# Kernel tuning notes

Measured on AMD Instinct MI355X. Metric: run time of the kernel, lower is better.

Reference implementation:

```python
import jax, jax.numpy as jnp
import numpy as np

D_MODEL = 1024
N_HEADS = 16
D_HEAD = D_MODEL // N_HEADS
D_FF = 4096
EPS = 1e-5


def layernorm(x, gamma, beta):
    mu = jnp.mean(x, axis=-1, keepdims=True)
    var = jnp.var(x, axis=-1, keepdims=True)
    return (x - mu) * jax.lax.rsqrt(var + EPS) * gamma + beta


def setup_inputs() -> dict:
    key = jax.random.key(0)
    ks = jax.random.split(key, 16)
    B, T = 4, 2048
    s = 1.0 / np.sqrt(D_MODEL)
    sf = 1.0 / np.sqrt(D_FF)
    return {
        "x": jax.random.normal(ks[0], (B, T, D_MODEL), jnp.float32),
        "gate_score": jax.random.uniform(ks[1], (B,), jnp.float32),
        "Wq": jax.random.normal(ks[2], (D_MODEL, D_MODEL), jnp.float32) * s,
        "bq": jnp.zeros((D_MODEL,), jnp.float32),
        "Wk": jax.random.normal(ks[3], (D_MODEL, D_MODEL), jnp.float32) * s,
        "bk": jnp.zeros((D_MODEL,), jnp.float32),
        "Wv": jax.random.normal(ks[4], (D_MODEL, D_MODEL), jnp.float32) * s,
        "bv": jnp.zeros((D_MODEL,), jnp.float32),
        "Wo": jax.random.normal(ks[5], (D_MODEL, D_MODEL), jnp.float32) * s,
        "bo": jnp.zeros((D_MODEL,), jnp.float32),
        "W1": jax.random.normal(ks[6], (D_MODEL, D_FF), jnp.float32) * s,
        "b1": jnp.zeros((D_FF,), jnp.float32),
        "W2": jax.random.normal(ks[7], (D_FF, D_MODEL), jnp.float32) * sf,
        "b2": jnp.zeros((D_MODEL,), jnp.float32),
        "gamma1": jnp.ones((D_MODEL,), jnp.float32),
        "beta1": jnp.zeros((D_MODEL,), jnp.float32),
        "gamma2": jnp.ones((D_MODEL,), jnp.float32),
        "beta2": jnp.zeros((D_MODEL,), jnp.float32),
    }


def reference(x, gate_score, Wq, bq, Wk, bk, Wv, bv, Wo, bo,
              W1, b1, W2, b2, gamma1, beta1, gamma2, beta2):
    B, T, C = x.shape
    # --- attention sub-block (pre-norm) ---
    h = layernorm(x, gamma1, beta1)
    Q = (h @ Wq + bq).reshape(B, T, N_HEADS, D_HEAD).transpose(0, 2, 1, 3)
    K = (h @ Wk + bk).reshape(B, T, N_HEADS, D_HEAD).transpose(0, 2, 1, 3)
    V = (h @ Wv + bv).reshape(B, T, N_HEADS, D_HEAD).transpose(0, 2, 1, 3)
    scores = jnp.einsum("bhqd,bhkd->bhqk", Q, K) / np.sqrt(D_HEAD)
    causal = jnp.tril(jnp.ones((T, T), dtype=bool))  # True = keep
    scores = jnp.where(causal, scores, -jnp.inf)
    attn = jax.nn.softmax(scores, axis=-1)
    ctx = jnp.einsum("bhqk,bhkd->bhqd", attn, V)
    ctx = ctx.transpose(0, 2, 1, 3).reshape(B, T, C)
    attn_out = ctx @ Wo + bo
    x1 = x + attn_out
    # --- FFN sub-block (pre-norm) ---
    h2 = layernorm(x1, gamma2, beta2)
    ff = jax.nn.gelu(h2 @ W1 + b1, approximate=False) @ W2 + b2
    x2 = x1 + ff
    # --- gated residual ---
    g = gate_score[:, None, None]
    return x + g * (x2 - x)
```

## Files before the change

### kernel.cpp

```cpp
#include <hip/hip_runtime.h>
#include <hip/hip_bf16.h>
#include <cmath>

typedef unsigned short u16;
typedef __attribute__((ext_vector_type(8))) short short8;
typedef __attribute__((ext_vector_type(4))) float f32x4;

#define DM 1024
#define NH 16
#define DH 64
#define DFF 4096
#define BB 4
#define TT 2048
#define MROWS (BB*TT)

__device__ __forceinline__ float bu2f(u16 u) {
    union { float f; unsigned v; } c; c.v = ((unsigned)u) << 16; return c.f;
}
__device__ __forceinline__ u16 f2bu(float f) {
    __hip_bfloat16 h = __float2bfloat16(f);
    union { __hip_bfloat16 h; u16 u; } c; c.h = h; return c.u;
}
__device__ __forceinline__ void async_copy16(const u16* g, u16* l) {
    __builtin_amdgcn_global_load_lds((const __attribute__((address_space(1))) void*)g,
                                     (__attribute__((address_space(3))) void*)l, 16, 0, 0);
}

__global__ void ln_kernel(const float* __restrict__ x, const float* __restrict__ gamma,
                          const float* __restrict__ beta, u16* __restrict__ out)
{
    int row = blockIdx.x;
    int tid = threadIdx.x;
    float4 v4 = ((const float4*)(x + (size_t)row * DM))[tid];
    float v[4] = { v4.x, v4.y, v4.z, v4.w };
    float s = v[0] + v[1] + v[2] + v[3];
    float ss = v[0]*v[0] + v[1]*v[1] + v[2]*v[2] + v[3]*v[3];
    #pragma unroll
    for (int o = 32; o > 0; o >>= 1) { s += __shfl_down(s, o); ss += __shfl_down(ss, o); }
    __shared__ float red[8];
    int w = tid >> 6;
    if ((tid & 63) == 0) { red[w] = s; red[4 + w] = ss; }
    __syncthreads();
    s  = red[0] + red[1] + red[2] + red[3];
    ss = red[4] + red[5] + red[6] + red[7];
    float mu  = s * (1.0f / DM);
    float var = ss * (1.0f / DM) - mu * mu;
    float rstd = rsqrtf(var + 1e-5f);
    float4 g4 = ((const float4*)gamma)[tid];
    float4 b4 = ((const float4*)beta)[tid];
    float g[4] = { g4.x, g4.y, g4.z, g4.w };
    float b[4] = { b4.x, b4.y, b4.z, b4.w };
    ushort4 o4;
    u16* op = (u16*)&o4;
    #pragma unroll
    for (int i = 0; i < 4; i++) op[i] = f2bu((v[i] - mu) * rstd * g[i] + b[i]);
    ((ushort4*)(out + (size_t)row * DM))[tid] = o4;
}

__global__ void transpose4_f2b(const float* __restrict__ w0, const float* __restrict__ w1,
                               const float* __restrict__ w2, const float* __restrict__ w3,
                               u16* __restrict__ outQKV, u16* __restrict__ outO)
{
    __shared__ u16 tile[32][33];
    const float* in = (blockIdx.z == 0) ? w0 : (blockIdx.z == 1) ? w1
                     : (blockIdx.z == 2) ? w2 : w3;
    u16* out = (blockIdx.z < 3) ? (outQKV + (size_t)blockIdx.z * DM * DM) : outO;
    int bx = blockIdx.x * 32;
    int by = blockIdx.y * 32;
    int tx = threadIdx.x, ty = threadIdx.y;
    #pragma unroll
    for (int i = 0; i < 32; i += 8)
        tile[ty + i][tx] = f2bu(in[(size_t)(by + ty + i) * DM + bx + tx]);
    __syncthreads();
    #pragma unroll
    for (int i = 0; i < 32; i += 8)
        out[(size_t)(bx + ty + i) * DM + by + tx] = tile[tx][ty + i];
}

__global__ void transpose_f2b(const float* __restrict__ in, u16* __restrict__ out,
                              int R, int C)
{
    __shared__ u16 tile[32][33];
    int bx = blockIdx.x * 32;
    int by = blockIdx.y * 32;
    int tx = threadIdx.x, ty = threadIdx.y;
    #pragma unroll
    for (int i = 0; i < 32; i += 8)
        tile[ty + i][tx] = f2bu(in[(size_t)(by + ty + i) * C + bx + tx]);
    __syncthreads();
    #pragma unroll
    for (int i = 0; i < 32; i += 8)
        out[(size_t)(bx + ty + i) * R + by + tx] = tile[tx][ty + i];
}

#define BM 128
#define BN 128
#define BK 64

template<int EPI>
__global__ void gemm_bt(
    const u16* __restrict__ A, const u16* __restrict__ Bt,
    const float* __restrict__ bias, const float* __restrict__ bias2,
    const float* __restrict__ bias3, void* __restrict__ Cv,
    const float* __restrict__ res, const float* __restrict__ x0,
    const float* __restrict__ gate, int M, int N, int K)
{
    __shared__ __align__(16) u16 As[BM * BK];
    __shared__ __align__(16) u16 Bs[BN * BK];
    int tid = threadIdx.x;
    int lane = tid & 63, wave = tid >> 6;
    int wm = (wave & 1) * 64, wn = (wave >> 1) * 64;
    int lm = lane & 15, quad = lane >> 4;
    size_t row0 = (size_t)blockIdx.x * BM;
    size_t col0 = (size_t)blockIdx.y * BN;

    int sr = tid >> 3;
    int scol = (((tid & 7) ^ (sr & 7)) * 8);
    const u16* Ag = A  + (row0 + sr) * (size_t)K + scol;
    const u16* Bg = Bt + (col0 + sr) * (size_t)K + scol;
    u16* Asl = As + tid * 8;
    u16* Bsl = Bs + tid * 8;

    int fc0 = ((0 * 4 + quad) ^ (lm & 7)) * 8;
    int fc1 = ((1 * 4 + quad) ^ (lm & 7)) * 8;

    f32x4 acc[4][4];
    #pragma unroll
    for (int i = 0; i < 4; i++)
        #pragma unroll
        for (int j = 0; j < 4; j++)
            acc[i][j] = (f32x4){0.f, 0.f, 0.f, 0.f};

    for (int k0 = 0; k0 < K; k0 += BK) {
        __syncthreads();
        async_copy16(Ag + k0,                  Asl);
        async_copy16(Ag + (size_t)32 * K + k0, Asl + 32 * BK);
        async_copy16(Ag + (size_t)64 * K + k0, Asl + 64 * BK);
        async_copy16(Ag + (size_t)96 * K + k0, Asl + 96 * BK);
        async_copy16(Bg + k0,                  Bsl);
        async_copy16(Bg + (size_t)32 * K + k0, Bsl + 32 * BK);
        async_copy16(Bg + (size_t)64 * K + k0, Bsl + 64 * BK);
        async_copy16(Bg + (size_t)96 * K + k0, Bsl + 96 * BK);
        __syncthreads();
        #pragma unroll
        for (int ks = 0; ks < 2; ks++) {
            int fc = ks ? fc1 : fc0;
            short8 af[4], bfr[4];
            #pragma unroll
            for (int t = 0; t < 4; t++) {
                af[t]  = *(const short8*)&As[(wm + t * 16 + lm) * BK + fc];
                bfr[t] = *(const short8*)&Bs[(wn + t * 16 + lm) * BK + fc];
            }
            #pragma unroll
            for (int mt = 0; mt < 4; mt++)
                #pragma unroll
                for (int nt = 0; nt < 4; nt++)
                    acc[mt][nt] = __builtin_amdgcn_mfma_f32_16x16x32_bf16(
                        af[mt], bfr[nt], acc[mt][nt], 0, 0, 0);
        }
    }

    u16*   C16 = (u16*)Cv;
    float* Cf  = (float*)Cv;

    const float* bb = bias;
    size_t csub = 0;
    if (EPI == 0 && bias2 != nullptr) {
        size_t cbase = col0 + wn;
        if (cbase >= 2048)      { bb = bias3; csub = 2048; }
        else if (cbase >= 1024) { bb = bias2; csub = 1024; }
    }

    #pragma unroll
    for (int mt = 0; mt < 4; mt++) {
        #pragma unroll
        for (int nt = 0; nt < 4; nt++) {
            #pragma unroll
            for (int r = 0; r < 4; r++) {
                size_t row = row0 + wm + mt * 16 + quad * 4 + r;
                size_t col = col0 + wn + nt * 16 + lm;
                size_t idx = row * (size_t)N + col;
                float v = acc[mt][nt][r] + bb[col - csub];
                if (EPI == 0) {
                    C16[idx] = f2bu(v);
                } else if (EPI == 1) {
                    Cf[idx] = v + res[idx];
                } else if (EPI == 2) {
                    v = 0.5f * v * (1.0f + erff(v * 0.70710678118f));
                    C16[idx] = f2bu(v);
                } else {
                    float xv  = x0[idx];
                    float x1v = res[idx];
                    float g   = gate[row >> 11];
                    Cf[idx] = xv + g * (x1v + v - xv);
                }
            }
        }
    }
}

#define AVS 72

__global__ __launch_bounds__(256, 4) void attn_mfma(
    const u16* __restrict__ QKV, u16* __restrict__ ctx)
{
    __shared__ __align__(16) u16 Kl[64][AVS];
    __shared__ __align__(16) u16 Vt[64][AVS];
    __shared__ __align__(16) u16 Pl[4][16][AVS];

    const int LD = 3 * DM;
    int tid = threadIdx.x, lane = tid & 63, w = tid >> 6;
    int lm = lane & 15, quad = lane >> 4;

    int bi = blockIdx.x;
    int pair = bi & 15, h = (bi >> 4) & 15, b = bi >> 8;
    int t1 = 31 - pair, t2 = pair;

    const size_t hoff = (size_t)h * DH;
    const u16* Qp = QKV + (size_t)b * TT * LD + hoff;
    const u16* Kp = Qp + DM;
    const u16* Vp = Qp + 2 * DM;

    short8 aqA[2], aqB[2];
    #pragma unroll
    for (int dc = 0; dc < 2; dc++) {
        aqA[dc] = *(const short8*)(Qp + (size_t)(t1 * 64 + w * 16 + lm) * LD + dc * 32 + quad * 8);
        aqB[dc] = *(const short8*)(Qp + (size_t)(t2 * 64 + w * 16 + lm) * LD + dc * 32 + quad * 8);
    }

    int kkey = tid & 63, kdim = (tid >> 6) * 16;
    int vkey = (tid & 31) * 2, vdim = (tid >> 5) * 8;

    const u16* kb0 = Kp + (size_t)kkey * LD + kdim;
    const u16* vb0 = Vp + (size_t)vkey * LD + vdim;
    const u16* vb1 = Vp + (size_t)(vkey + 1) * LD + vdim;

    const float sc = 0.18033688011f;
    const float FM = 24.0f;
    const short s1 = (short)0x3F80;
    const short8 ones = (short8){s1, s1, s1, s1, s1, s1, s1, s1};

    uint4 kr0 = *(const uint4*)(kb0);
    uint4 kr1 = *(const uint4*)(kb0 + 8);
    uint4 vr0 = *(const uint4*)(vb0);
    uint4 vr1 = *(const uint4*)(vb1);

    #pragma unroll
    for (int ti = 0; ti < 2; ti++) {
        int tcur = (ti == 0) ? t1 : t2;
        int nch = tcur + 1;
        int q0 = tcur * 64;
        int qw = q0 + w * 16;
        short8 a0 = (ti == 0) ? aqA[0] : aqB[0];
        short8 a1 = (ti == 0) ? aqA[1] : aqB[1];
        int qv = qw + lm;

        f32x4 o[4], o5;
        #pragma unroll
        for (int ds = 0; ds < 4; ds++) o[ds] = (f32x4){0.f, 0.f, 0.f, 0.f};
        o5 = (f32x4){0.f, 0.f, 0.f, 0.f};

        for (int c = 0; c < nch; c++) {
            int kb = c * 64;
            __syncthreads();
            *(uint4*)&Kl[kkey][kdim]     = kr0;
            *(uint4*)&Kl[kkey][kdim + 8] = kr1;
            {
                const u16* p0 = (const u16*)&vr0;
                const u16* p1 = (const u16*)&vr1;
                #pragma unroll
                for (int j = 0; j < 8; j++) {
                    ushort2 pk = { p0[j], p1[j] };
                    *(ushort2*)&Vt[vdim + j][vkey] = pk;
                }
            }
            __syncthreads();

            {
                size_t offn = (c + 1 < nch) ? (size_t)(c + 1) * 64 * LD : 0;
                kr0 = *(const uint4*)(kb0 + offn);
                kr1 = *(const uint4*)(kb0 + offn + 8);
                vr0 = *(const uint4*)(vb0 + offn);
                vr1 = *(const uint4*)(vb1 + offn);
            }

            f32x4 s[4];
            #pragma unroll
            for (int ks = 0; ks < 4; ks++) s[ks] = (f32x4){0.f, 0.f, 0.f, 0.f};
            #pragma unroll
            for (int ks = 0; ks < 4; ks++) {
                short8 k0 = *(const short8*)&Kl[ks * 16 + lm][quad * 8];
                short8 k1 = *(const short8*)&Kl[ks * 16 + lm][32 + quad * 8];
                s[ks] = __builtin_amdgcn_mfma_f32_16x16x32_bf16(k0, a0, s[ks], 0, 0, 0);
                s[ks] = __builtin_amdgcn_mfma_f32_16x16x32_bf16(k1, a1, s[ks], 0, 0, 0);
            }

            bool mz = (kb + 63 > qw);
            #pragma unroll
            for (int ks = 0; ks < 4; ks++) {
                int kbase = kb + ks * 16 + quad * 4;
                ushort4 pk;
                u16* pp = (u16*)&pk;
                #pragma unroll
                for (int r = 0; r < 4; r++) {
                    float v = s[ks][r] * sc - FM;
                    if (mz && (kbase + r > qv)) v = -INFINITY;
                    pp[r] = f2bu(exp2f(v));
                }
                *(ushort4*)&Pl[w][lm][ks * 16 + quad * 4] = pk;
            }

            #pragma unroll
            for (int kc = 0; kc < 2; kc++) {
                short8 ap = *(const short8*)&Pl[w][lm][kc * 32 + quad * 8];
                #pragma unroll
                for (int ds = 0; ds < 4; ds++) {
                    short8 bv = *(const short8*)&Vt[ds * 16 + lm][kc * 32 + quad * 8];
                    o[ds] = __builtin_amdgcn_mfma_f32_16x16x32_bf16(ap, bv, o[ds], 0, 0, 0);
                }
                o5 = __builtin_amdgcn_mfma_f32_16x16x32_bf16(ap, ones, o5, 0, 0, 0);
            }
        }

        float inv[4];
        #pragma unroll
        for (int r = 0; r < 4; r++) inv[r] = 1.0f / o5[r];
        #pragma unroll
        for (int ds = 0; ds < 4; ds++)
            #pragma unroll
            for (int r = 0; r < 4; r++) {
                size_t row = (size_t)(b * TT + qw + quad * 4 + r);
                ctx[row * DM + hoff + ds * 16 + lm] = f2bu(o[ds][r] * inv[r]);
            }
    }
}

extern "C" void kernel_launch(void* const* d_in, const int* in_sizes, int n_in,
                              void* d_out, int out_size, void* d_ws, size_t ws_size,
                              hipStream_t stream)
{
    const float* x    = (const float*)d_in[0];
    const float* gate = (const float*)d_in[1];
    const float* Wq   = (const float*)d_in[2];
    const float* bq   = (const float*)d_in[3];
    const float* Wk   = (const float*)d_in[4];
    const float* bk   = (const float*)d_in[5];
    const float* Wv   = (const float*)d_in[6];
    const float* bv   = (const float*)d_in[7];
    const float* Wo   = (const float*)d_in[8];
    const float* bo   = (const float*)d_in[9];
    const float* W1   = (const float*)d_in[10];
    const float* b1   = (const float*)d_in[11];
    const float* W2   = (const float*)d_in[12];
    const float* b2   = (const float*)d_in[13];
    const float* gamma1 = (const float*)d_in[14];
    const float* beta1  = (const float*)d_in[15];
    const float* gamma2 = (const float*)d_in[16];
    const float* beta2  = (const float*)d_in[17];
    float* out = (float*)d_out;

    char* ws = (char*)d_ws;
    const size_t MB = 1024 * 1024;
    u16* WtQKV = (u16*)(ws + 0 * MB);
    u16* WtO   = (u16*)(ws + 6 * MB);
    u16* Wt1   = (u16*)(ws + 8 * MB);
    u16* Wt2   = (u16*)(ws + 16 * MB);
    u16* h     = (u16*)(ws + 24 * MB);
    u16* ctx   = (u16*)(ws + 24 * MB);
    u16* QKVb  = (u16*)(ws + 40 * MB);
    float* x1  = (float*)(ws + 40 * MB);
    u16* h2    = (u16*)(ws + 72 * MB);
    u16* ff    = (u16*)(ws + 88 * MB);

    dim3 tb(32, 8);
    transpose4_f2b<<<dim3(32, 32, 4), tb, 0, stream>>>(Wq, Wk, Wv, Wo, WtQKV, WtO);
    transpose_f2b<<<dim3(DFF / 32, DM / 32), tb, 0, stream>>>(W1, Wt1, DM, DFF);
    transpose_f2b<<<dim3(DM / 32, DFF / 32), tb, 0, stream>>>(W2, Wt2, DFF, DM);

    ln_kernel<<<MROWS, 256, 0, stream>>>(x, gamma1, beta1, h);

    gemm_bt<0><<<dim3(MROWS / BM, 3 * DM / BN), 256, 0, stream>>>(
        h, WtQKV, bq, bk, bv, QKVb, nullptr, nullptr, nullptr, MROWS, 3 * DM, DM);

    attn_mfma<<<BB * NH * 16, 256, 0, stream>>>(QKVb, ctx);

    gemm_bt<1><<<dim3(MROWS / BM, DM / BN), 256, 0, stream>>>(
        ctx, WtO, bo, nullptr, nullptr, x1, x, nullptr, nullptr, MROWS, DM, DM);

    ln_kernel<<<MROWS, 256, 0, stream>>>(x1, gamma2, beta2, h2);

    gemm_bt<2><<<dim3(MROWS / BM, DFF / BN), 256, 0, stream>>>(
        h2, Wt1, b1, nullptr, nullptr, ff, nullptr, nullptr, nullptr, MROWS, DFF, DM);

    gemm_bt<3><<<dim3(MROWS / BM, DM / BN), 256, 0, stream>>>(
        ff, Wt2, b2, nullptr, nullptr, out, x1, x, gate, MROWS, DM, DFF);
}
```

Measured before the change: 537.4 us.

## Share K/V tile loads between both query tiles in causal attention

Each attention block handles a pair of query tiles (t1 = 31-pair and t2 = pair). It now walks the key chunks once for the longer tile and runs the shorter tile's compute on the same staged K/V tiles while c <= t2, instead of looping over K/V twice. This removes the redundant global loads, LDS staging and barriers for the shorter tile. The cost is two sets of output accumulators held live, which raises register pressure and may lower occupancy.

Result: slower. 794.9 us (+47.9%).

```diff
diff --git a/kernel.cpp b/kernel.cpp
--- a/kernel.cpp
+++ b/kernel.cpp
@@ -221,11 +221,14 @@
     const u16* Kp = Qp + DM;
     const u16* Vp = Qp + 2 * DM;
 
-    short8 aqA[2], aqB[2];
+    int qw1 = t1 * 64 + w * 16, qv1 = qw1 + lm;
+    int qw2 = t2 * 64 + w * 16, qv2 = qw2 + lm;
+
+    short8 aq1[2], aq2[2];
     #pragma unroll
     for (int dc = 0; dc < 2; dc++) {
-        aqA[dc] = *(const short8*)(Qp + (size_t)(t1 * 64 + w * 16 + lm) * LD + dc * 32 + quad * 8);
-        aqB[dc] = *(const short8*)(Qp + (size_t)(t2 * 64 + w * 16 + lm) * LD + dc * 32 + quad * 8);
+        aq1[dc] = *(const short8*)(Qp + (size_t)(qw1 + lm) * LD + dc * 32 + quad * 8);
+        aq2[dc] = *(const short8*)(Qp + (size_t)(qw2 + lm) * LD + dc * 32 + quad * 8);
     }
 
     int kkey = tid & 63, kdim = (tid >> 6) * 16;
@@ -240,97 +243,109 @@
     const short s1 = (short)0x3F80;
     const short8 ones = (short8){s1, s1, s1, s1, s1, s1, s1, s1};
 
+    f32x4 o1[4], o2[4], l1, l2;
+    #pragma unroll
+    for (int ds = 0; ds < 4; ds++) {
+        o1[ds] = (f32x4){0.f, 0.f, 0.f, 0.f};
+        o2[ds] = (f32x4){0.f, 0.f, 0.f, 0.f};
+    }
+    l1 = (f32x4){0.f, 0.f, 0.f, 0.f};
+    l2 = (f32x4){0.f, 0.f, 0.f, 0.f};
+
     uint4 kr0 = *(const uint4*)(kb0);
     uint4 kr1 = *(const uint4*)(kb0 + 8);
     uint4 vr0 = *(const uint4*)(vb0);
     uint4 vr1 = *(const uint4*)(vb1);
 
-    #pragma unroll
-    for (int ti = 0; ti < 2; ti++) {
-        int tcur = (ti == 0) ? t1 : t2;
-        int nch = tcur + 1;
-        int q0 = tcur * 64;
-        int qw = q0 + w * 16;
-        short8 a0 = (ti == 0) ? aqA[0] : aqB[0];
-        short8 a1 = (ti == 0) ? aqA[1] : aqB[1];
-        int qv = qw + lm;
-
-        f32x4 o[4], o5;
-        #pragma unroll
-        for (int ds = 0; ds < 4; ds++) o[ds] = (f32x4){0.f, 0.f, 0.f, 0.f};
-        o5 = (f32x4){0.f, 0.f, 0.f, 0.f};
-
-        for (int c = 0; c < nch; c++) {
-            int kb = c * 64;
-            __syncthreads();
-            *(uint4*)&Kl[kkey][kdim]     = kr0;
-            *(uint4*)&Kl[kkey][kdim + 8] = kr1;
-            {
-                const u16* p0 = (const u16*)&vr0;
-                const u16* p1 = (const u16*)&vr1;
-                #pragma unroll
-                for (int j = 0; j < 8; j++) {
-                    ushort2 pk = { p0[j], p1[j] };
-                    *(ushort2*)&Vt[vdim + j][vkey] = pk;
-                }
-            }
-            __syncthreads();
-
-            {
-                size_t offn = (c + 1 < nch) ? (size_t)(c + 1) * 64 * LD : 0;
-                kr0 = *(const uint4*)(kb0 + offn);
-                kr1 = *(const uint4*)(kb0 + offn + 8);
-                vr0 = *(const uint4*)(vb0 + offn);
-                vr1 = *(const uint4*)(vb1 + offn);
-            }
-
-            f32x4 s[4];
-            #pragma unroll
-            for (int ks = 0; ks < 4; ks++) s[ks] = (f32x4){0.f, 0.f, 0.f, 0.f};
-            #pragma unroll
-            for (int ks = 0; ks < 4; ks++) {
-                short8 k0 = *(const short8*)&Kl[ks * 16 + lm][quad * 8];
-                short8 k1 = *(const short8*)&Kl[ks * 16 + lm][32 + quad * 8];
-                s[ks] = __builtin_amdgcn_mfma_f32_16x16x32_bf16(k0, a0, s[ks], 0, 0, 0);
-                s[ks] = __builtin_amdgcn_mfma_f32_16x16x32_bf16(k1, a1, s[ks], 0, 0, 0);
-            }
-
-            bool mz = (kb + 63 > qw);
-            #pragma unroll
-            for (int ks = 0; ks < 4; ks++) {
-                int kbase = kb + ks * 16 + quad * 4;
-                ushort4 pk;
-                u16* pp = (u16*)&pk;
-                #pragma unroll
-                for (int r = 0; r < 4; r++) {
-                    float v = s[ks][r] * sc - FM;
-                    if (mz && (kbase + r > qv)) v = -INFINITY;
-                    pp[r] = f2bu(exp2f(v));
-                }
-                *(ushort4*)&Pl[w][lm][ks * 16 + quad * 4] = pk;
-            }
-
-            #pragma unroll
-            for (int kc = 0; kc < 2; kc++) {
-                short8 ap = *(const short8*)&Pl[w][lm][kc * 32 + quad * 8];
-                #pragma unroll
-                for (int ds = 0; ds < 4; ds++) {
-                    short8 bv = *(const short8*)&Vt[ds * 16 + lm][kc * 32 + quad * 8];
-                    o[ds] = __builtin_amdgcn_mfma_f32_16x16x32_bf16(ap, bv, o[ds], 0, 0, 0);
-                }
-                o5 = __builtin_amdgcn_mfma_f32_16x16x32_bf16(ap, ones, o5, 0, 0, 0);
-            }
-        }
-
+    auto tile_step = [&](short8 a0, short8 a1, int qw, int qv, int kb,
+                         f32x4 (&o)[4], f32x4& l) {
+        f32x4 s[4];
+        #pragma unroll
+        for (int ks = 0; ks < 4; ks++) s[ks] = (f32x4){0.f, 0.f, 0.f, 0.f};
+        #pragma unroll
+        for (int ks = 0; ks < 4; ks++) {
+            short8 k0 = *(const short8*)&Kl[ks * 16 + lm][quad * 8];
+            short8 k1 = *(const short8*)&Kl[ks * 16 + lm][32 + quad * 8];
+            s[ks] = __builtin_amdgcn_mfma_f32_16x16x32_bf16(k0, a0, s[ks], 0, 0, 0);
+            s[ks] = __builtin_amdgcn_mfma_f32_16x16x32_bf16(k1, a1, s[ks], 0, 0, 0);
+        }
+
+        bool mz = (kb + 63 > qw);
+        #pragma unroll
+        for (int ks = 0; ks < 4; ks++) {
+            int kbase = kb + ks * 16 + quad * 4;
+            ushort4 pk;
+            u16* pp = (u16*)&pk;
+            #pragma unroll
+            for (int r = 0; r < 4; r++) {
+                float v = s[ks][r] * sc - FM;
+                if (mz && (kbase + r > qv)) v = -INFINITY;
+                pp[r] = f2bu(exp2f(v));
+            }
+            *(ushort4*)&Pl[w][lm][ks * 16 + quad * 4] = pk;
+        }
+
+        #pragma unroll
+        for (int kc = 0; kc < 2; kc++) {
+            short8 ap = *(const short8*)&Pl[w][lm][kc * 32 + quad * 8];
+            #pragma unroll
+            for (int ds = 0; ds < 4; ds++) {
+                short8 bv = *(const short8*)&Vt[ds * 16 + lm][kc * 32 + quad * 8];
+                o[ds] = __builtin_amdgcn_mfma_f32_16x16x32_bf16(ap, bv, o[ds], 0, 0, 0);
+            }
+            l = __builtin_amdgcn_mfma_f32_16x16x32_bf16(ap, ones, l, 0, 0, 0);
+        }
+    };
+
+    int nch = t1 + 1;
+    for (int c = 0; c < nch; c++) {
+        int kb = c * 64;
+        __syncthreads();
+        *(uint4*)&Kl[kkey][kdim]     = kr0;
+        *(uint4*)&Kl[kkey][kdim + 8] = kr1;
+        {
+            const u16* p0 = (const u16*)&vr0;
+            const u16* p1 = (const u16*)&vr1;
+            #pragma unroll
+            for (int j = 0; j < 8; j++) {
+                ushort2 pk = { p0[j], p1[j] };
+                *(ushort2*)&Vt[vdim + j][vkey] = pk;
+            }
+        }
+        __syncthreads();
+
+        {
+            size_t offn = (c + 1 < nch) ? (size_t)(c + 1) * 64 * LD : 0;
+            kr0 = *(const uint4*)(kb0 + offn);
+            kr1 = *(const uint4*)(kb0 + offn + 8);
+            vr0 = *(const uint4*)(vb0 + offn);
+            vr1 = *(const uint4*)(vb1 + offn);
+        }
+
+        tile_step(aq1[0], aq1[1], qw1, qv1, kb, o1, l1);
+        if (c <= t2)
+            tile_step(aq2[0], aq2[1], qw2, qv2, kb, o2, l2);
+    }
+
+    {
         float inv[4];
         #pragma unroll
-        for (int r = 0; r < 4; r++) inv[r] = 1.0f / o5[r];
+        for (int r = 0; r < 4; r++) inv[r] = 1.0f / l1[r];
         #pragma unroll
         for (int ds = 0; ds < 4; ds++)
             #pragma unroll
             for (int r = 0; r < 4; r++) {
-                size_t row = (size_t)(b * TT + qw + quad * 4 + r);
-                ctx[row * DM + hoff + ds * 16 + lm] = f2bu(o[ds][r] * inv[r]);
+                size_t row = (size_t)(b * TT + qw1 + quad * 4 + r);
+                ctx[row * DM + hoff + ds * 16 + lm] = f2bu(o1[ds][r] * inv[r]);
+            }
+        #pragma unroll
+        for (int r = 0; r < 4; r++) inv[r] = 1.0f / l2[r];
+        #pragma unroll
+        for (int ds = 0; ds < 4; ds++)
+            #pragma unroll
+            for (int r = 0; r < 4; r++) {
+                size_t row = (size_t)(b * TT + qw2 + quad * 4 + r);
+                ctx[row * DM + hoff + ds * 16 + lm] = f2bu(o2[ds][r] * inv[r]);
             }
     }
 }
```

## Rewrite causal attention with 32x32 MFMA, key-split waves and swizzled LDS

Applied to the files above, without the earlier changes.

The attention kernel now has each block handle one 64-query tile instead of a pair of tiles, and the grid doubles to compensate. The block ID is remapped so the longest tiles are scheduled first. Waves are arranged as 2 query groups by 2 key halves and use 32x32x16 bf16 MFMAs. Probabilities stay in registers, with a cross-half lane shuffle instead of a round trip through LDS. The row sum is accumulated in scalar code instead of with a ones-MFMA, and K/V use XOR-swizzled LDS without padding. The two key-half partial outputs are reduced through LDS at the end. This aims to cut LDS traffic and bank conflicts and to raise MFMA efficiency, at the cost of a final cross-wave reduction and some idle waves on diagonal tiles.

New measurement: 557.3 us. 1.04x slower.

```diff
diff --git a/kernel.cpp b/kernel.cpp
--- a/kernel.cpp
+++ b/kernel.cpp
@@ -5,6 +5,7 @@
 typedef unsigned short u16;
 typedef __attribute__((ext_vector_type(8))) short short8;
 typedef __attribute__((ext_vector_type(4))) float f32x4;
+typedef __attribute__((ext_vector_type(16))) float f32x16;
 
 #define DM 1024
 #define NH 16
@@ -199,139 +200,186 @@
     }
 }
 
-#define AVS 72
 
 __global__ __launch_bounds__(256, 4) void attn_mfma(
     const u16* __restrict__ QKV, u16* __restrict__ ctx)
 {
-    __shared__ __align__(16) u16 Kl[64][AVS];
-    __shared__ __align__(16) u16 Vt[64][AVS];
-    __shared__ __align__(16) u16 Pl[4][16][AVS];
+    __shared__ __align__(16) u16 KV[2][64][64];
+    __shared__ float Ls[2][32];
 
     const int LD = 3 * DM;
     int tid = threadIdx.x, lane = tid & 63, w = tid >> 6;
-    int lm = lane & 15, quad = lane >> 4;
-
-    int bi = blockIdx.x;
-    int pair = bi & 15, h = (bi >> 4) & 15, b = bi >> 8;
-    int t1 = 31 - pair, t2 = pair;
+    int qgrp = w & 1, kg = w >> 1;
+    int l31 = lane & 31, hi = lane >> 5;
+
+    unsigned orig = blockIdx.x;
+    int bi = (int)((orig & 7) * 256 + (orig >> 3));
+    int b = bi >> 9, h = (bi >> 5) & 15, t = 31 - (bi & 31);
 
     const size_t hoff = (size_t)h * DH;
     const u16* Qp = QKV + (size_t)b * TT * LD + hoff;
     const u16* Kp = Qp + DM;
     const u16* Vp = Qp + 2 * DM;
 
-    short8 aqA[2], aqB[2];
-    #pragma unroll
-    for (int dc = 0; dc < 2; dc++) {
-        aqA[dc] = *(const short8*)(Qp + (size_t)(t1 * 64 + w * 16 + lm) * LD + dc * 32 + quad * 8);
-        aqB[dc] = *(const short8*)(Qp + (size_t)(t2 * 64 + w * 16 + lm) * LD + dc * 32 + quad * 8);
-    }
-
-    int kkey = tid & 63, kdim = (tid >> 6) * 16;
+    int q0 = t * 64 + qgrp * 32;
+
+    short8 aq0 = *(const short8*)(Qp + (size_t)(q0 + l31) * LD +  0 + hi * 8);
+    short8 aq1 = *(const short8*)(Qp + (size_t)(q0 + l31) * LD + 16 + hi * 8);
+    short8 aq2 = *(const short8*)(Qp + (size_t)(q0 + l31) * LD + 32 + hi * 8);
+    short8 aq3 = *(const short8*)(Qp + (size_t)(q0 + l31) * LD + 48 + hi * 8);
+
+    int kkey = tid & 63, kw = tid >> 6;
     int vkey = (tid & 31) * 2, vdim = (tid >> 5) * 8;
 
-    const u16* kb0 = Kp + (size_t)kkey * LD + kdim;
+    const u16* kb0 = Kp + (size_t)kkey * LD + kw * 16;
     const u16* vb0 = Vp + (size_t)vkey * LD + vdim;
     const u16* vb1 = Vp + (size_t)(vkey + 1) * LD + vdim;
 
+    u16 (*Kl)[64] = KV[0];
+    u16 (*Vt)[64] = KV[1];
+
+    int ksw0 = ((kw * 2)     ^ (kkey & 7)) * 8;
+    int ksw1 = ((kw * 2 + 1) ^ (kkey & 7)) * 8;
+    int vc8 = vkey >> 3, vlo = vkey & 7;
+
     const float sc = 0.18033688011f;
     const float FM = 24.0f;
-    const short s1 = (short)0x3F80;
-    const short8 ones = (short8){s1, s1, s1, s1, s1, s1, s1, s1};
+
+    f32x16 o0, o1;
+    #pragma unroll
+    for (int j = 0; j < 16; j++) { o0[j] = 0.f; o1[j] = 0.f; }
+    float lac = 0.f;
 
     uint4 kr0 = *(const uint4*)(kb0);
     uint4 kr1 = *(const uint4*)(kb0 + 8);
     uint4 vr0 = *(const uint4*)(vb0);
     uint4 vr1 = *(const uint4*)(vb1);
 
-    #pragma unroll
-    for (int ti = 0; ti < 2; ti++) {
-        int tcur = (ti == 0) ? t1 : t2;
-        int nch = tcur + 1;
-        int q0 = tcur * 64;
-        int qw = q0 + w * 16;
-        short8 a0 = (ti == 0) ? aqA[0] : aqB[0];
-        short8 a1 = (ti == 0) ? aqA[1] : aqB[1];
-        int qv = qw + lm;
-
-        f32x4 o[4], o5;
+    int krow = kg * 32 + l31;
+    int kx = krow & 7;
+    int r7 = l31 & 7;
+
+    for (int c = 0; c <= t; c++) {
+        __syncthreads();
+        *(uint4*)&Kl[kkey][ksw0] = kr0;
+        *(uint4*)&Kl[kkey][ksw1] = kr1;
+        {
+            const u16* p0 = (const u16*)&vr0;
+            const u16* p1 = (const u16*)&vr1;
+            #pragma unroll
+            for (int j = 0; j < 8; j++) {
+                ushort2 pk = { p0[j], p1[j] };
+                *(ushort2*)&Vt[vdim + j][((vc8 ^ j) * 8) + vlo] = pk;
+            }
+        }
+        __syncthreads();
+
+        {
+            size_t offn = (c < t) ? (size_t)(c + 1) * 64 * LD : 0;
+            kr0 = *(const uint4*)(kb0 + offn);
+            kr1 = *(const uint4*)(kb0 + offn + 8);
+            vr0 = *(const uint4*)(vb0 + offn);
+            vr1 = *(const uint4*)(vb1 + offn);
+        }
+
+        int kb = c * 64;
+        bool active = (kb + kg * 32) <= (q0 + 31);
+        if (active) {
+            f32x16 s;
+            #pragma unroll
+            for (int j = 0; j < 16; j++) s[j] = 0.f;
+            {
+                short8 kf0 = *(const short8*)&Kl[krow][((0 + hi) ^ kx) * 8];
+                s = __builtin_amdgcn_mfma_f32_32x32x16_bf16(kf0, aq0, s, 0, 0, 0);
+                short8 kf1 = *(const short8*)&Kl[krow][((2 + hi) ^ kx) * 8];
+                s = __builtin_amdgcn_mfma_f32_32x32x16_bf16(kf1, aq1, s, 0, 0, 0);
+                short8 kf2 = *(const short8*)&Kl[krow][((4 + hi) ^ kx) * 8];
+                s = __builtin_amdgcn_mfma_f32_32x32x16_bf16(kf2, aq2, s, 0, 0, 0);
+                short8 kf3 = *(const short8*)&Kl[krow][((6 + hi) ^ kx) * 8];
+                s = __builtin_amdgcn_mfma_f32_32x32x16_bf16(kf3, aq3, s, 0, 0, 0);
+            }
+
+            float p[16];
+            bool need_mask = (c == t) && (kg == qgrp);
+            if (!need_mask) {
+                #pragma unroll
+                for (int rg = 0; rg < 16; rg++)
+                    p[rg] = exp2f(fmaf(s[rg], sc, -FM));
+            } else {
+                #pragma unroll
+                for (int rg = 0; rg < 16; rg++) {
+                    int klocal = (rg & 3) + 8 * (rg >> 2) + 4 * hi;
+                    float v = fmaf(s[rg], sc, -FM);
+                    if (klocal > l31) v = -INFINITY;
+                    p[rg] = exp2f(v);
+                }
+            }
+            lac += ((p[0] + p[1]) + (p[2] + p[3])) + ((p[4] + p[5]) + (p[6] + p[7]))
+                 + ((p[8] + p[9]) + (p[10] + p[11])) + ((p[12] + p[13]) + (p[14] + p[15]));
+
+            unsigned pk0[4], pk1[4];
+            #pragma unroll
+            for (int g = 0; g < 4; g++) {
+                asm("v_cvt_pk_bf16_f32 %0, %1, %2" : "=v"(pk0[g]) : "v"(p[4*g]),   "v"(p[4*g+1]));
+                asm("v_cvt_pk_bf16_f32 %0, %1, %2" : "=v"(pk1[g]) : "v"(p[4*g+2]), "v"(p[4*g+3]));
+            }
+
+            #pragma unroll
+            for (int kc = 0; kc < 2; kc++) {
+                unsigned own0 = hi ? pk0[2*kc+1] : pk0[2*kc];
+                unsigned own1 = hi ? pk1[2*kc+1] : pk1[2*kc];
+                unsigned snd0 = hi ? pk0[2*kc]   : pk0[2*kc+1];
+                unsigned snd1 = hi ? pk1[2*kc]   : pk1[2*kc+1];
+                unsigned rc0 = (unsigned)__shfl_xor((int)snd0, 32);
+                unsigned rc1 = (unsigned)__shfl_xor((int)snd1, 32);
+                union { uint4 u; short8 s8; } bw;
+                bw.u.x = hi ? rc0 : own0;
+                bw.u.y = hi ? rc1 : own1;
+                bw.u.z = hi ? own0 : rc0;
+                bw.u.w = hi ? own1 : rc1;
+                int vcol = ((kg * 4 + kc * 2 + hi) ^ r7) * 8;
+                short8 v0 = *(const short8*)&Vt[l31][vcol];
+                short8 v1 = *(const short8*)&Vt[32 + l31][vcol];
+                o0 = __builtin_amdgcn_mfma_f32_32x32x16_bf16(v0, bw.s8, o0, 0, 0, 0);
+                o1 = __builtin_amdgcn_mfma_f32_32x32x16_bf16(v1, bw.s8, o1, 0, 0, 0);
+            }
+        }
+    }
+
+    lac += __shfl_xor(lac, 32);
+    __syncthreads();
+    float* Ol = (float*)&KV[0][0][0];
+    if (kg == 0) {
         #pragma unroll
-        for (int ds = 0; ds < 4; ds++) o[ds] = (f32x4){0.f, 0.f, 0.f, 0.f};
-        o5 = (f32x4){0.f, 0.f, 0.f, 0.f};
-
-        for (int c = 0; c < nch; c++) {
-            int kb = c * 64;
-            __syncthreads();
-            *(uint4*)&Kl[kkey][kdim]     = kr0;
-            *(uint4*)&Kl[kkey][kdim + 8] = kr1;
-            {
-                const u16* p0 = (const u16*)&vr0;
-                const u16* p1 = (const u16*)&vr1;
-                #pragma unroll
-                for (int j = 0; j < 8; j++) {
-                    ushort2 pk = { p0[j], p1[j] };
-                    *(ushort2*)&Vt[vdim + j][vkey] = pk;
-                }
-            }
-            __syncthreads();
-
-            {
-                size_t offn = (c + 1 < nch) ? (size_t)(c + 1) * 64 * LD : 0;
-                kr0 = *(const uint4*)(kb0 + offn);
-                kr1 = *(const uint4*)(kb0 + offn + 8);
-                vr0 = *(const uint4*)(vb0 + offn);
-                vr1 = *(const uint4*)(vb1 + offn);
-            }
-
-            f32x4 s[4];
-            #pragma unroll
-            for (int ks = 0; ks < 4; ks++) s[ks] = (f32x4){0.f, 0.f, 0.f, 0.f};
-            #pragma unroll
-            for (int ks = 0; ks < 4; ks++) {
-                short8 k0 = *(const short8*)&Kl[ks * 16 + lm][quad * 8];
-                short8 k1 = *(const short8*)&Kl[ks * 16 + lm][32 + quad * 8];
-                s[ks] = __builtin_amdgcn_mfma_f32_16x16x32_bf16(k0, a0, s[ks], 0, 0, 0);
-                s[ks] = __builtin_amdgcn_mfma_f32_16x16x32_bf16(k1, a1, s[ks], 0, 0, 0);
-            }
-
-            bool mz = (kb + 63 > qw);
-            #pragma unroll
-            for (int ks = 0; ks < 4; ks++) {
-                int kbase = kb + ks * 16 + quad * 4;
-                ushort4 pk;
-                u16* pp = (u16*)&pk;
+        for (int rg = 0; rg < 16; rg++) {
+            int dim = (rg & 3) + 8 * (rg >> 2) + 4 * hi;
+            Ol[qgrp * 2048 + dim * 32 + l31]        = o0[rg];
+            Ol[qgrp * 2048 + (32 + dim) * 32 + l31] = o1[rg];
+        }
+        if (hi == 0) Ls[qgrp][l31] = lac;
+    }
+    __syncthreads();
+    if (kg == 1) {
+        float ltot = lac + Ls[qgrp][l31];
+        float inv = 1.0f / ltot;
+        size_t rowbase = ((size_t)(b * TT + q0 + l31)) * DM + hoff;
+        #pragma unroll
+        for (int dg = 0; dg < 2; dg++) {
+            #pragma unroll
+            for (int g = 0; g < 4; g++) {
+                ushort4 o4;
+                u16* op = (u16*)&o4;
                 #pragma unroll
                 for (int r = 0; r < 4; r++) {
-                    float v = s[ks][r] * sc - FM;
-                    if (mz && (kbase + r > qv)) v = -INFINITY;
-                    pp[r] = f2bu(exp2f(v));
+                    int rg = 4 * g + r;
+                    int dim = dg * 32 + 8 * g + 4 * hi + r;
+                    float part = dg ? o1[rg] : o0[rg];
+                    float val = (part + Ol[qgrp * 2048 + dim * 32 + l31]) * inv;
+                    op[r] = f2bu(val);
                 }
-                *(ushort4*)&Pl[w][lm][ks * 16 + quad * 4] = pk;
-            }
-
-            #pragma unroll
-            for (int kc = 0; kc < 2; kc++) {
-                short8 ap = *(const short8*)&Pl[w][lm][kc * 32 + quad * 8];
-                #pragma unroll
-                for (int ds = 0; ds < 4; ds++) {
-                    short8 bv = *(const short8*)&Vt[ds * 16 + lm][kc * 32 + quad * 8];
-                    o[ds] = __builtin_amdgcn_mfma_f32_16x16x32_bf16(ap, bv, o[ds], 0, 0, 0);
-                }
-                o5 = __builtin_amdgcn_mfma_f32_16x16x32_bf16(ap, ones, o5, 0, 0, 0);
-            }
-        }
-
-        float inv[4];
-        #pragma unroll
-        for (int r = 0; r < 4; r++) inv[r] = 1.0f / o5[r];
-        #pragma unroll
-        for (int ds = 0; ds < 4; ds++)
-            #pragma unroll
-            for (int r = 0; r < 4; r++) {
-                size_t row = (size_t)(b * TT + qw + quad * 4 + r);
-                ctx[row * DM + hoff + ds * 16 + lm] = f2bu(o[ds][r] * inv[r]);
-            }
+                *(ushort4*)(ctx + rowbase + dg * 32 + 8 * g + 4 * hi) = o4;
+            }
+        }
     }
 }
 
@@ -382,7 +430,7 @@
     gemm_bt<0><<<dim3(MROWS / BM, 3 * DM / BN), 256, 0, stream>>>(
         h, WtQKV, bq, bk, bv, QKVb, nullptr, nullptr, nullptr, MROWS, 3 * DM, DM);
 
-    attn_mfma<<<BB * NH * 16, 256, 0, stream>>>(QKVb, ctx);
+    attn_mfma<<<BB * NH * 32, 256, 0, stream>>>(QKVb, ctx);
 
     gemm_bt<1><<<dim3(MROWS / BM, DM / BN), 256, 0, stream>>>(
         ctx, WtO, bo, nullptr, nullptr, x1, x, nullptr, nullptr, MROWS, DM, DM);
```

## Add 256x256-tile 8-wave GEMM with quadrant ping-pong pipeline for QKV and FFN1

Applied to the files above, without the earlier changes.

Adds a new bf16 GEMM kernel with 256x256 block tiles, 512 threads, and double-buffered LDS split into quadrants. Global-to-LDS async loads for the next k-step are interleaved with MFMA work on each quadrant, with wave priority raised around the MFMA bursts. The kernel is used for the QKV projection and the first FFN GEMM. The larger tiles cut global traffic per FLOP, at the cost of more registers, heavier barrier synchronisation, and fewer blocks in flight.

After: 552.3 us. +2.8%, slower.

```diff
diff --git a/kernel.cpp b/kernel.cpp
--- a/kernel.cpp
+++ b/kernel.cpp
@@ -194,6 +194,193 @@
                     float g   = gate[row >> 11];
                     Cf[idx] = xv + g * (x1v + v - xv);
                 }
+            }
+        }
+    }
+}
+
+#define BM2 256
+#define BN2 256
+#define BK2 64
+
+template<int EPI>
+__global__ __launch_bounds__(512, 2) void gemm_bt256(
+    const u16* __restrict__ A, const u16* __restrict__ Bt,
+    const float* __restrict__ bias, const float* __restrict__ bias2,
+    const float* __restrict__ bias3, void* __restrict__ Cv,
+    int M, int N, int K)
+{
+    __shared__ __align__(16) u16 LA[2][2][128][64];
+    __shared__ __align__(16) u16 LB[2][2][128][64];
+
+    int tid = threadIdx.x;
+    int lane = tid & 63, wave = tid >> 6;
+    int wm = wave >> 2, wn = wave & 3;
+    int lm = lane & 15, quad = lane >> 4;
+
+    size_t row0 = (size_t)blockIdx.x * BM2;
+    size_t col0 = (size_t)blockIdx.y * BN2;
+
+    int srow = wave * 8 + (lane >> 3);
+    int scol = ((lane & 7) ^ ((lane >> 3) & 7)) * 8;
+    const u16* Ag = A  + (row0 + srow) * (size_t)K + scol;
+    const u16* Bg = Bt + (col0 + srow) * (size_t)K + scol;
+
+    int fc0 = (quad ^ (lm & 7)) * 8;
+    int fc1 = ((4 + quad) ^ (lm & 7)) * 8;
+
+    f32x4 acc[8][4];
+    #pragma unroll
+    for (int i = 0; i < 8; i++)
+        #pragma unroll
+        for (int j = 0; j < 4; j++)
+            acc[i][j] = (f32x4){0.f, 0.f, 0.f, 0.f};
+
+    const int NT = K / BK2;
+
+    async_copy16(Ag,                   &LA[0][0][0][0]  + tid * 8);
+    async_copy16(Ag + (size_t)64 * K,  &LA[0][0][64][0] + tid * 8);
+    async_copy16(Bg,                   &LB[0][0][0][0]  + tid * 8);
+    async_copy16(Bg + (size_t)64 * K,  &LB[0][0][64][0] + tid * 8);
+    async_copy16(Bg + (size_t)128 * K, &LB[0][1][0][0]  + tid * 8);
+    async_copy16(Bg + (size_t)192 * K, &LB[0][1][64][0] + tid * 8);
+    async_copy16(Ag + (size_t)128 * K, &LA[0][1][0][0]  + tid * 8);
+    async_copy16(Ag + (size_t)192 * K, &LA[0][1][64][0] + tid * 8);
+    asm volatile("s_waitcnt vmcnt(4)" ::: "memory");
+    __builtin_amdgcn_s_barrier();
+    __builtin_amdgcn_sched_barrier(0);
+
+    for (int t = 0; t < NT; ++t) {
+        int cur = t & 1, nb = cur ^ 1;
+        bool hn = (t + 1 < NT);
+        size_t koff = (size_t)(t + 1) * BK2;
+
+        short8 af[4][2], bf[2][2], bg[2][2];
+
+        #pragma unroll
+        for (int mf = 0; mf < 4; mf++) {
+            af[mf][0] = *(const short8*)&LA[cur][0][wm * 64 + mf * 16 + lm][fc0];
+            af[mf][1] = *(const short8*)&LA[cur][0][wm * 64 + mf * 16 + lm][fc1];
+        }
+        #pragma unroll
+        for (int nf = 0; nf < 2; nf++) {
+            bf[nf][0] = *(const short8*)&LB[cur][0][wn * 32 + nf * 16 + lm][fc0];
+            bf[nf][1] = *(const short8*)&LB[cur][0][wn * 32 + nf * 16 + lm][fc1];
+        }
+        if (hn) {
+            async_copy16(Ag + koff,                   &LA[nb][0][0][0]  + tid * 8);
+            async_copy16(Ag + (size_t)64 * K + koff,  &LA[nb][0][64][0] + tid * 8);
+            asm volatile("s_waitcnt vmcnt(4)" ::: "memory");
+        } else {
+            asm volatile("s_waitcnt vmcnt(2)" ::: "memory");
+        }
+        __builtin_amdgcn_s_barrier();
+        __builtin_amdgcn_sched_barrier(0);
+        __builtin_amdgcn_s_setprio(1);
+        #pragma unroll
+        for (int mf = 0; mf < 4; mf++)
+            #pragma unroll
+            for (int nf = 0; nf < 2; nf++) {
+                acc[mf][nf] = __builtin_amdgcn_mfma_f32_16x16x32_bf16(af[mf][0], bf[nf][0], acc[mf][nf], 0, 0, 0);
+                acc[mf][nf] = __builtin_amdgcn_mfma_f32_16x16x32_bf16(af[mf][1], bf[nf][1], acc[mf][nf], 0, 0, 0);
+            }
+        __builtin_amdgcn_s_setprio(0);
+        __builtin_amdgcn_s_barrier();
+        __builtin_amdgcn_sched_barrier(0);
+
+        #pragma unroll
+        for (int nf = 0; nf < 2; nf++) {
+            bg[nf][0] = *(const short8*)&LB[cur][1][wn * 32 + nf * 16 + lm][fc0];
+            bg[nf][1] = *(const short8*)&LB[cur][1][wn * 32 + nf * 16 + lm][fc1];
+        }
+        if (hn) {
+            async_copy16(Bg + koff,                   &LB[nb][0][0][0]  + tid * 8);
+            async_copy16(Bg + (size_t)64 * K + koff,  &LB[nb][0][64][0] + tid * 8);
+            asm volatile("s_waitcnt vmcnt(4)" ::: "memory");
+        } else {
+            asm volatile("s_waitcnt vmcnt(0)" ::: "memory");
+        }
+        __builtin_amdgcn_s_barrier();
+        __builtin_amdgcn_sched_barrier(0);
+        __builtin_amdgcn_s_setprio(1);
+        #pragma unroll
+        for (int mf = 0; mf < 4; mf++)
+            #pragma unroll
+            for (int nf = 0; nf < 2; nf++) {
+                acc[mf][2 + nf] = __builtin_amdgcn_mfma_f32_16x16x32_bf16(af[mf][0], bg[nf][0], acc[mf][2 + nf], 0, 0, 0);
+                acc[mf][2 + nf] = __builtin_amdgcn_mfma_f32_16x16x32_bf16(af[mf][1], bg[nf][1], acc[mf][2 + nf], 0, 0, 0);
+            }
+        __builtin_amdgcn_s_setprio(0);
+        __builtin_amdgcn_s_barrier();
+        __builtin_amdgcn_sched_barrier(0);
+
+        #pragma unroll
+        for (int mf = 0; mf < 4; mf++) {
+            af[mf][0] = *(const short8*)&LA[cur][1][wm * 64 + mf * 16 + lm][fc0];
+            af[mf][1] = *(const short8*)&LA[cur][1][wm * 64 + mf * 16 + lm][fc1];
+        }
+        if (hn) {
+            async_copy16(Bg + (size_t)128 * K + koff, &LB[nb][1][0][0]  + tid * 8);
+            async_copy16(Bg + (size_t)192 * K + koff, &LB[nb][1][64][0] + tid * 8);
+        }
+        __builtin_amdgcn_s_barrier();
+        __builtin_amdgcn_sched_barrier(0);
+        __builtin_amdgcn_s_setprio(1);
+        #pragma unroll
+        for (int mf = 0; mf < 4; mf++)
+            #pragma unroll
+            for (int nf = 0; nf < 2; nf++) {
+                acc[4 + mf][2 + nf] = __builtin_amdgcn_mfma_f32_16x16x32_bf16(af[mf][0], bg[nf][0], acc[4 + mf][2 + nf], 0, 0, 0);
+                acc[4 + mf][2 + nf] = __builtin_amdgcn_mfma_f32_16x16x32_bf16(af[mf][1], bg[nf][1], acc[4 + mf][2 + nf], 0, 0, 0);
+            }
+        __builtin_amdgcn_s_setprio(0);
+        __builtin_amdgcn_s_barrier();
+        __builtin_amdgcn_sched_barrier(0);
+
+        #pragma unroll
+        for (int nf = 0; nf < 2; nf++) {
+            bf[nf][0] = *(const short8*)&LB[cur][0][wn * 32 + nf * 16 + lm][fc0];
+            bf[nf][1] = *(const short8*)&LB[cur][0][wn * 32 + nf * 16 + lm][fc1];
+        }
+        if (hn) {
+            async_copy16(Ag + (size_t)128 * K + koff, &LA[nb][1][0][0]  + tid * 8);
+            async_copy16(Ag + (size_t)192 * K + koff, &LA[nb][1][64][0] + tid * 8);
+            asm volatile("s_waitcnt vmcnt(4)" ::: "memory");
+        }
+        __builtin_amdgcn_s_barrier();
+        __builtin_amdgcn_sched_barrier(0);
+        __builtin_amdgcn_s_setprio(1);
+        #pragma unroll
+        for (int mf = 0; mf < 4; mf++)
+            #pragma unroll
+            for (int nf = 0; nf < 2; nf++) {
+                acc[4 + mf][nf] = __builtin_amdgcn_mfma_f32_16x16x32_bf16(af[mf][0], bf[nf][0], acc[4 + mf][nf], 0, 0, 0);
+                acc[4 + mf][nf] = __builtin_amdgcn_mfma_f32_16x16x32_bf16(af[mf][1], bf[nf][1], acc[4 + mf][nf], 0, 0, 0);
+            }
+        __builtin_amdgcn_s_setprio(0);
+        __builtin_amdgcn_s_barrier();
+        __builtin_amdgcn_sched_barrier(0);
+    }
+
+    u16* C16 = (u16*)Cv;
+    const float* bb = bias;
+    size_t csub = 0;
+    if (EPI == 0 && bias2 != nullptr) {
+        if (col0 >= 2048)      { bb = bias3; csub = 2048; }
+        else if (col0 >= 1024) { bb = bias2; csub = 1024; }
+    }
+    #pragma unroll
+    for (int mq = 0; mq < 8; mq++) {
+        #pragma unroll
+        for (int nq = 0; nq < 4; nq++) {
+            #pragma unroll
+            for (int r = 0; r < 4; r++) {
+                size_t row = row0 + (size_t)(mq >> 2) * 128 + wm * 64 + (mq & 3) * 16 + quad * 4 + r;
+                size_t col = col0 + (size_t)(nq >> 1) * 128 + wn * 32 + (nq & 1) * 16 + lm;
+                float v = acc[mq][nq][r] + bb[col - csub];
+                if (EPI == 2)
+                    v = 0.5f * v * (1.0f + erff(v * 0.70710678118f));
+                C16[row * (size_t)N + col] = f2bu(v);
             }
         }
     }
@@ -379,8 +566,8 @@
 
     ln_kernel<<<MROWS, 256, 0, stream>>>(x, gamma1, beta1, h);
 
-    gemm_bt<0><<<dim3(MROWS / BM, 3 * DM / BN), 256, 0, stream>>>(
-        h, WtQKV, bq, bk, bv, QKVb, nullptr, nullptr, nullptr, MROWS, 3 * DM, DM);
+    gemm_bt256<0><<<dim3(MROWS / BM2, 3 * DM / BN2), 512, 0, stream>>>(
+        h, WtQKV, bq, bk, bv, QKVb, MROWS, 3 * DM, DM);
 
     attn_mfma<<<BB * NH * 16, 256, 0, stream>>>(QKVb, ctx);
 
@@ -389,8 +576,8 @@
 
     ln_kernel<<<MROWS, 256, 0, stream>>>(x1, gamma2, beta2, h2);
 
-    gemm_bt<2><<<dim3(MROWS / BM, DFF / BN), 256, 0, stream>>>(
-        h2, Wt1, b1, nullptr, nullptr, ff, nullptr, nullptr, nullptr, MROWS, DFF, DM);
+    gemm_bt256<2><<<dim3(MROWS / BM2, DFF / BN2), 512, 0, stream>>>(
+        h2, Wt1, b1, nullptr, nullptr, ff, MROWS, DFF, DM);
 
     gemm_bt<3><<<dim3(MROWS / BM, DM / BN), 256, 0, stream>>>(
         ff, Wt2, b2, nullptr, nullptr, out, x1, x, gate, MROWS, DM, DFF);
```
